# Kernel tuning notes

Hardware: AMD Instinct MI355X
Metric: run time of the kernel (lower is better)

## Reference

```python
import jax, jax.numpy as jnp
import numpy as np

D = 768      # qkv.in_features (ViT-Base)
R = 16       # LoRA rank
T = 8        # task_id: number of previously saved adapters
B_, S_ = 32, 256
TAU = 1.0


def setup_inputs() -> dict:
    key = jax.random.key(0)
    ks = jax.random.split(key, 13)
    s = lambda k, shape, sc=0.02: jax.random.normal(k, shape, jnp.float32) * sc
    return {
        "x": jax.random.normal(ks[0], (B_, S_, D), jnp.float32),
        "qkv_w": s(ks[1], (3 * D, D)),           # torch Linear weight [out,in]
        "qkv_b": s(ks[2], (3 * D,)),
        "la_q": s(ks[3], (R, D)),                # current-task LoRA A_q [r,d]
        "lb_q": s(ks[4], (D, R)),                # current-task LoRA B_q [d,r]
        "la_v": s(ks[5], (R, D)),
        "lb_v": s(ks[6], (D, R)),
        "A_q": s(ks[7], (T, R, D)),              # saved per-task A_q stacks
        "B_q": s(ks[8], (T, D, R)),
        "A_v": s(ks[9], (T, R, D)),
        "B_v": s(ks[10], (T, D, R)),
        "gate_logits": jax.random.normal(ks[11], (T,), jnp.float32),
        "alpha": jnp.ones((T + 1,), jnp.float32),  # gumbel_gate.alpha, indexed by task_id
    }


def _moe_branch(x, A, B, beta):
    """Weighted sum over T tasks of (x @ A_t^T @ B_t^T) / (||A_t||*||B_t||), weight beta_t.

    Vectorizes the per-task serial low-rank matmuls of the torch loop into two
    batched einsums; beta/norm scaling is folded into B to avoid materializing
    per-task [B,S,D] outputs.
    """
    nA = jnp.sqrt(jnp.sum(A * A, axis=(1, 2)))   # [T] Frobenius norms
    nB = jnp.sqrt(jnp.sum(B * B, axis=(1, 2)))
    scale = beta / (nA * nB)                      # [T]
    za = jnp.einsum('bsd,trd->bstr', x, A)       # [B,S,T,r]
    Bs = B * scale[:, None, None]                 # [T,D,r]
    return jnp.einsum('bstr,tdr->bsd', za, Bs)   # [B,S,D]


def _lora(x, a, b):
    # torch: b(a(x)) with Linear weights a:[r,d], b:[d,r]
    return jnp.einsum('bsr,dr->bsd', jnp.einsum('bsd,rd->bsr', x, a), b)


def reference(x, qkv_w, qkv_b, la_q, lb_q, la_v, lb_v, A_q, B_q, A_v, B_v, gate_logits, alpha):
    # Gumbel-softmax gate over tasks (deterministic/eval path: softmax(logits/tau), hard=False)
    beta = jax.nn.softmax(gate_logits / TAU)
    a_cur = alpha[T]  # alpha[self.task_id]
    new_q = _moe_branch(x, A_q, B_q, beta) + a_cur * _lora(x, la_q, lb_q)
    new_v = _moe_branch(x, A_v, B_v, beta) + a_cur * _lora(x, la_v, lb_v)
    qkv = jnp.einsum('bsd,ed->bse', x, qkv_w) + qkv_b  # [B,S,3D]
    qkv = qkv.at[..., :D].add(new_q)
    qkv = qkv.at[..., 2 * D:].add(new_v)
    return qkv
```

## Files before the change

kernel.cpp:

```cpp
#include <hip/hip_runtime.h>

#define TOK 8192
#define DD  768
#define NOUT 2304
#define TT  8
#define RR  16
#define KRANK 144

typedef __bf16 bf16;
typedef __bf16 bf16x4 __attribute__((ext_vector_type(4)));
typedef __bf16 bf16x8 __attribute__((ext_vector_type(8)));
typedef float  floatx4 __attribute__((ext_vector_type(4)));

__device__ __forceinline__ void gl_lds16(const void* g, void* l) {
    __builtin_amdgcn_global_load_lds((const __attribute__((address_space(1))) void*)g,
                                     (__attribute__((address_space(3))) void*)l, 16, 0, 0);
}

__global__ __launch_bounds__(256) void prep_kernel(
    const float* __restrict__ A_q, const float* __restrict__ B_q,
    const float* __restrict__ A_v, const float* __restrict__ B_v,
    const float* __restrict__ x, bf16* __restrict__ xb,
    float* __restrict__ norms)
{
    __shared__ float ws4[4];
    const int b = blockIdx.x;
    if (b < 32) {
        const float* base;
        switch (b >> 3) {
            case 0: base = A_q; break;
            case 1: base = B_q; break;
            case 2: base = A_v; break;
            default: base = B_v; break;
        }
        base += (b & 7) * (RR * DD);
        float s = 0.f;
        for (int i = threadIdx.x; i < RR * DD; i += 256) {
            float v = base[i];
            s = fmaf(v, v, s);
        }
        #pragma unroll
        for (int off = 32; off > 0; off >>= 1) s += __shfl_down(s, off);
        if ((threadIdx.x & 63) == 0) ws4[threadIdx.x >> 6] = s;
        __syncthreads();
        if (threadIdx.x == 0)
            norms[b] = sqrtf(ws4[0] + ws4[1] + ws4[2] + ws4[3]);
    } else {
        const int idx = ((b - 32) * 256 + threadIdx.x) * 4;
        const float4 v = *(const float4*)(x + idx);
        bf16x4 o = { (bf16)v.x, (bf16)v.y, (bf16)v.z, (bf16)v.w };
        *(bf16x4*)(xb + idx) = o;
    }
}

__global__ __launch_bounds__(256) void fold_kernel(
    const float* __restrict__ qkv_w,
    const float* __restrict__ A_q, const float* __restrict__ la_q,
    const float* __restrict__ B_q, const float* __restrict__ lb_q,
    const float* __restrict__ A_v, const float* __restrict__ la_v,
    const float* __restrict__ B_v, const float* __restrict__ lb_v,
    const float* __restrict__ gate_logits, const float* __restrict__ alpha,
    const float* __restrict__ norms, bf16* __restrict__ Wc)
{
    const int tid = threadIdx.x;
    const int d = blockIdx.x * 256 + tid;
    const int gy = blockIdx.y;

    if (gy >= 96 && gy < 192) {
        const int rowbase = DD + (gy - 96) * 8;
        #pragma unroll
        for (int j = 0; j < 8; ++j) {
            const int row = rowbase + j;
            Wc[row * DD + d] = (bf16)qkv_w[row * DD + d];
        }
        return;
    }

    __shared__ float c_lds[8 * KRANK];
    __shared__ float sc_sh[TT];
    __shared__ float acur_sh;

    const bool is_v = (gy >= 192);
    const int e0 = (is_v ? gy - 192 : gy) * 8;
    const float* Astack = is_v ? A_v : A_q;
    const float* la     = is_v ? la_v : la_q;
    const float* Bmat   = is_v ? B_v : B_q;
    const float* lb     = is_v ? lb_v : lb_q;
    const float* nA     = norms + (is_v ? 16 : 0);
    const float* nB     = norms + (is_v ? 24 : 8);
    const int rowbase   = (is_v ? 2 * DD : 0) + e0;

    if (tid == 0) {
        float mx = gate_logits[0];
        for (int t = 1; t < TT; ++t) mx = fmaxf(mx, gate_logits[t]);
        float e[TT], s = 0.f;
        for (int t = 0; t < TT; ++t) { e[t] = __expf(gate_logits[t] - mx); s += e[t]; }
        for (int t = 0; t < TT; ++t) sc_sh[t] = (e[t] / s) / (nA[t] * nB[t]);
        acur_sh = alpha[TT];
    }
    __syncthreads();

    for (int idx = tid; idx < 8 * KRANK; idx += 256) {
        const int j = idx / KRANK, i = idx - j * KRANK;
        const int e = e0 + j;
        float v;
        if (i < TT * RR) {
            const int t = i >> 4, r = i & 15;
            v = sc_sh[t] * Bmat[(t * DD + e) * RR + r];
        } else {
            v = acur_sh * lb[e * RR + (i - TT * RR)];
        }
        c_lds[j * KRANK + i] = v;
    }
    __syncthreads();

    float acc[8] = {0.f, 0.f, 0.f, 0.f, 0.f, 0.f, 0.f, 0.f};

    for (int i = 0; i < TT * RR; i += 4) {
        const float a0 = Astack[(i + 0) * DD + d];
        const float a1 = Astack[(i + 1) * DD + d];
        const float a2 = Astack[(i + 2) * DD + d];
        const float a3 = Astack[(i + 3) * DD + d];
        #pragma unroll
        for (int j = 0; j < 8; ++j) {
            const float4 cv = *(const float4*)&c_lds[j * KRANK + i];
            acc[j] = fmaf(a0, cv.x, fmaf(a1, cv.y, fmaf(a2, cv.z, fmaf(a3, cv.w, acc[j]))));
        }
    }
    #pragma unroll
    for (int i = 0; i < RR; i += 4) {
        const float a0 = la[(i + 0) * DD + d];
        const float a1 = la[(i + 1) * DD + d];
        const float a2 = la[(i + 2) * DD + d];
        const float a3 = la[(i + 3) * DD + d];
        #pragma unroll
        for (int j = 0; j < 8; ++j) {
            const float4 cv = *(const float4*)&c_lds[j * KRANK + TT * RR + i];
            acc[j] = fmaf(a0, cv.x, fmaf(a1, cv.y, fmaf(a2, cv.z, fmaf(a3, cv.w, acc[j]))));
        }
    }

    #pragma unroll
    for (int j = 0; j < 8; ++j) {
        const int row = rowbase + j;
        Wc[row * DD + d] = (bf16)(qkv_w[row * DD + d] + acc[j]);
    }
}

__global__ __launch_bounds__(256, 2) void gemm_kernel(
    const bf16* __restrict__ A, const bf16* __restrict__ B,
    const float* __restrict__ bias, float* __restrict__ C)
{
    __shared__ bf16 lds_a[128 * 64];
    __shared__ bf16 lds_b[128 * 64];
    const int tid  = threadIdx.x;
    const int lane = tid & 63;
    const int wave = tid >> 6;

    const int flat  = blockIdx.y * gridDim.x + blockIdx.x;
    const int xcd   = flat & 7;
    const int local = flat >> 3;
    const int mb    = xcd * 8 + (local & 7);
    const int nb    = local >> 3;
    const int m0 = mb * 128;
    const int n0 = nb * 128;

    const int wm = (wave >> 1) * 64;
    const int wn = (wave & 1) * 64;

    const int srow = lane >> 3;
    const int scol = ((lane & 7) ^ srow) * 8;

    floatx4 acc[4][4];
    #pragma unroll
    for (int i = 0; i < 4; ++i)
        #pragma unroll
        for (int j = 0; j < 4; ++j)
            acc[i][j] = (floatx4){0.f, 0.f, 0.f, 0.f};

    for (int kt = 0; kt < DD / 64; ++kt) {
        const int k0 = kt * 64;
        #pragma unroll
        for (int i = 0; i < 4; ++i) {
            const int j = i * 4 + wave;
            const int row = j * 8 + srow;
            gl_lds16(A + (m0 + row) * DD + k0 + scol, &lds_a[j * 512]);
            gl_lds16(B + (n0 + row) * DD + k0 + scol, &lds_b[j * 512]);
        }
        __syncthreads();
        #pragma unroll
        for (int ks = 0; ks < 2; ++ks) {
            bf16x8 af[4], bfr[4];
            const int c_log = ks * 4 + (lane >> 4);
            #pragma unroll
            for (int mt = 0; mt < 4; ++mt) {
                const int r = wm + mt * 16 + (lane & 15);
                af[mt] = *(const bf16x8*)&lds_a[r * 64 + ((c_log ^ (r & 7)) * 8)];
            }
            #pragma unroll
            for (int nt = 0; nt < 4; ++nt) {
                const int r = wn + nt * 16 + (lane & 15);
                bfr[nt] = *(const bf16x8*)&lds_b[r * 64 + ((c_log ^ (r & 7)) * 8)];
            }
            #pragma unroll
            for (int mt = 0; mt < 4; ++mt)
                #pragma unroll
                for (int nt = 0; nt < 4; ++nt)
                    acc[mt][nt] = __builtin_amdgcn_mfma_f32_16x16x32_bf16(
                        af[mt], bfr[nt], acc[mt][nt], 0, 0, 0);
        }
        __syncthreads();
    }

    const int cr = (lane >> 4) * 4;
    const int cc = lane & 15;
    #pragma unroll
    for (int nt = 0; nt < 4; ++nt) {
        const int gn = n0 + wn + nt * 16 + cc;
        const float bv = bias[gn];
        #pragma unroll
        for (int mt = 0; mt < 4; ++mt) {
            const int gmb = m0 + wm + mt * 16 + cr;
            #pragma unroll
            for (int r = 0; r < 4; ++r)
                C[(gmb + r) * NOUT + gn] = acc[mt][nt][r] + bv;
        }
    }
}

extern "C" void kernel_launch(void* const* d_in, const int* in_sizes, int n_in,
                              void* d_out, int out_size, void* d_ws, size_t ws_size,
                              hipStream_t stream)
{
    const float* x           = (const float*)d_in[0];
    const float* qkv_w       = (const float*)d_in[1];
    const float* qkv_b       = (const float*)d_in[2];
    const float* la_q        = (const float*)d_in[3];
    const float* lb_q        = (const float*)d_in[4];
    const float* la_v        = (const float*)d_in[5];
    const float* lb_v        = (const float*)d_in[6];
    const float* A_q         = (const float*)d_in[7];
    const float* B_q         = (const float*)d_in[8];
    const float* A_v         = (const float*)d_in[9];
    const float* B_v         = (const float*)d_in[10];
    const float* gate_logits = (const float*)d_in[11];
    const float* alpha       = (const float*)d_in[12];
    float* out = (float*)d_out;

    char* ws = (char*)d_ws;
    bf16*  Xbf    = (bf16*)ws;
    bf16*  Wc     = (bf16*)(ws + 12582912);
    float* norms  = (float*)(ws + 12582912 + 3538944);

    prep_kernel<<<32 + TOK * DD / 1024, 256, 0, stream>>>(A_q, B_q, A_v, B_v,
                                                          x, Xbf, norms);
    fold_kernel<<<dim3(3, 288), 256, 0, stream>>>(qkv_w,
                                                  A_q, la_q, B_q, lb_q,
                                                  A_v, la_v, B_v, lb_v,
                                                  gate_logits, alpha, norms, Wc);
    gemm_kernel<<<dim3(NOUT / 128, TOK / 128), 256, 0, stream>>>(Xbf, Wc, qkv_b, out);
}
```

Before: 174.6 us.

## Double-buffer GEMM LDS tiles and stage output through LDS for coalesced stores

The bf16 GEMM main loop now ping-pongs between two LDS buffers, issuing the next k-tile's global-to-LDS loads before computing the current tile, which removes one barrier per iteration and overlaps loads with MFMA work. The epilogue writes the fp32 accumulator tile plus bias into LDS first, then each block writes it to global memory as row-contiguous float4 stores instead of scattered 4-byte stores. LDS use rises to 64 KB per block, which may limit the launch_bounds(256,2) occupancy target. There is also a possible race: no wait/barrier guards the async loads into the next buffer before it is read in the following iteration.

```diff
diff --git a/kernel.cpp b/kernel.cpp
--- a/kernel.cpp
+++ b/kernel.cpp
@@ -151,8 +151,8 @@
     const bf16* __restrict__ A, const bf16* __restrict__ B,
     const float* __restrict__ bias, float* __restrict__ C)
 {
-    __shared__ bf16 lds_a[128 * 64];
-    __shared__ bf16 lds_b[128 * 64];
+    __shared__ __align__(16) char smem[65536];
+
     const int tid  = threadIdx.x;
     const int lane = tid & 63;
     const int wave = tid >> 6;
@@ -178,16 +178,28 @@
         for (int j = 0; j < 4; ++j)
             acc[i][j] = (floatx4){0.f, 0.f, 0.f, 0.f};
 
-    for (int kt = 0; kt < DD / 64; ++kt) {
+    auto stage = [&](int kt, int buf) {
         const int k0 = kt * 64;
+        bf16* la = (bf16*)(smem + buf * 32768);
+        bf16* lb = (bf16*)(smem + buf * 32768 + 16384);
         #pragma unroll
         for (int i = 0; i < 4; ++i) {
             const int j = i * 4 + wave;
             const int row = j * 8 + srow;
-            gl_lds16(A + (m0 + row) * DD + k0 + scol, &lds_a[j * 512]);
-            gl_lds16(B + (n0 + row) * DD + k0 + scol, &lds_b[j * 512]);
-        }
-        __syncthreads();
+            gl_lds16(A + (m0 + row) * DD + k0 + scol, &la[j * 512]);
+            gl_lds16(B + (n0 + row) * DD + k0 + scol, &lb[j * 512]);
+        }
+    };
+
+    stage(0, 0);
+    __syncthreads();
+
+    int cur = 0;
+    for (int kt = 0; kt < DD / 64; ++kt) {
+        if (kt + 1 < DD / 64) stage(kt + 1, cur ^ 1);
+
+        const bf16* la = (const bf16*)(smem + cur * 32768);
+        const bf16* lb = (const bf16*)(smem + cur * 32768 + 16384);
         #pragma unroll
         for (int ks = 0; ks < 2; ++ks) {
             bf16x8 af[4], bfr[4];
@@ -195,12 +207,12 @@
             #pragma unroll
             for (int mt = 0; mt < 4; ++mt) {
                 const int r = wm + mt * 16 + (lane & 15);
-                af[mt] = *(const bf16x8*)&lds_a[r * 64 + ((c_log ^ (r & 7)) * 8)];
+                af[mt] = *(const bf16x8*)&la[r * 64 + ((c_log ^ (r & 7)) * 8)];
             }
             #pragma unroll
             for (int nt = 0; nt < 4; ++nt) {
                 const int r = wn + nt * 16 + (lane & 15);
-                bfr[nt] = *(const bf16x8*)&lds_b[r * 64 + ((c_log ^ (r & 7)) * 8)];
+                bfr[nt] = *(const bf16x8*)&lb[r * 64 + ((c_log ^ (r & 7)) * 8)];
             }
             #pragma unroll
             for (int mt = 0; mt < 4; ++mt)
@@ -210,21 +222,32 @@
                         af[mt], bfr[nt], acc[mt][nt], 0, 0, 0);
         }
         __syncthreads();
-    }
-
+        cur ^= 1;
+    }
+
+    float* ctile = (float*)smem;
     const int cr = (lane >> 4) * 4;
     const int cc = lane & 15;
     #pragma unroll
     for (int nt = 0; nt < 4; ++nt) {
-        const int gn = n0 + wn + nt * 16 + cc;
-        const float bv = bias[gn];
+        const int col = wn + nt * 16 + cc;
+        const float bv = bias[n0 + col];
         #pragma unroll
         for (int mt = 0; mt < 4; ++mt) {
-            const int gmb = m0 + wm + mt * 16 + cr;
+            const int rowb = wm + mt * 16 + cr;
             #pragma unroll
             for (int r = 0; r < 4; ++r)
-                C[(gmb + r) * NOUT + gn] = acc[mt][nt][r] + bv;
-        }
+                ctile[(rowb + r) * 128 + col] = acc[mt][nt][r] + bv;
+        }
+    }
+    __syncthreads();
+    #pragma unroll
+    for (int p = 0; p < 16; ++p) {
+        const int f   = p * 256 + tid;
+        const int row = f >> 5;
+        const int c4  = (f & 31) * 4;
+        const float4 v = *(const float4*)&ctile[row * 128 + c4];
+        *(float4*)&C[(m0 + row) * NOUT + n0 + c4] = v;
     }
 }
 
```

Result: no change. 175.1 us (+0.3%).

## Enlarge GEMM tile to 128x256 and double-buffer A with register-prefetched B

Applied to the files above, without the earlier changes.

The bf16 GEMM tile grows from 128x128 to 128x256. Each wave now owns a 64-wide column strip across all 128 rows, which improves operand reuse per LDS load. A tiles are double-buffered in LDS through async global-to-LDS loads, so the next k-step's load overlaps the current MFMAs. B tiles are prefetched into registers and written to a wave-private LDS region after compute, which removes one barrier per k-step. The cost is more accumulator registers and 64 KB of LDS per block, which may limit occupancy, and a 1D grid of 576 blocks with XCD-aware mapping.

```diff
diff --git a/kernel.cpp b/kernel.cpp
--- a/kernel.cpp
+++ b/kernel.cpp
@@ -6,6 +6,7 @@
 #define TT  8
 #define RR  16
 #define KRANK 144
+#define NKT  (DD / 64)
 
 typedef __bf16 bf16;
 typedef __bf16 bf16x4 __attribute__((ext_vector_type(4)));
@@ -151,65 +152,96 @@
     const bf16* __restrict__ A, const bf16* __restrict__ B,
     const float* __restrict__ bias, float* __restrict__ C)
 {
-    __shared__ bf16 lds_a[128 * 64];
-    __shared__ bf16 lds_b[128 * 64];
+    __shared__ __align__(16) char smem[65536];
+    bf16* const b_lds = (bf16*)(smem + 32768);
+
     const int tid  = threadIdx.x;
     const int lane = tid & 63;
     const int wave = tid >> 6;
 
-    const int flat  = blockIdx.y * gridDim.x + blockIdx.x;
+    const int flat  = blockIdx.x;
     const int xcd   = flat & 7;
     const int local = flat >> 3;
     const int mb    = xcd * 8 + (local & 7);
     const int nb    = local >> 3;
     const int m0 = mb * 128;
-    const int n0 = nb * 128;
-
-    const int wm = (wave >> 1) * 64;
-    const int wn = (wave & 1) * 64;
+    const int n0 = nb * 256;
+
+    const int wn = wave * 64;
 
     const int srow = lane >> 3;
-    const int scol = ((lane & 7) ^ srow) * 8;
-
-    floatx4 acc[4][4];
-    #pragma unroll
-    for (int i = 0; i < 4; ++i)
+    const int sxor = ((lane & 7) ^ srow) * 8;
+
+    const bf16* b_gbase = B + (n0 + wn + srow) * DD + sxor;
+    bf16* const b_wbase = b_lds + (wn + srow) * 64 + (lane & 7) * 8;
+
+    floatx4 acc[8][4];
+    #pragma unroll
+    for (int i = 0; i < 8; ++i)
         #pragma unroll
         for (int j = 0; j < 4; ++j)
             acc[i][j] = (floatx4){0.f, 0.f, 0.f, 0.f};
 
-    for (int kt = 0; kt < DD / 64; ++kt) {
+    uint4 breg[8];
+
+    auto stageA = [&](int kt, int buf) {
         const int k0 = kt * 64;
+        bf16* abuf = (bf16*)(smem + buf * 16384);
         #pragma unroll
         for (int i = 0; i < 4; ++i) {
             const int j = i * 4 + wave;
-            const int row = j * 8 + srow;
-            gl_lds16(A + (m0 + row) * DD + k0 + scol, &lds_a[j * 512]);
-            gl_lds16(B + (n0 + row) * DD + k0 + scol, &lds_b[j * 512]);
-        }
-        __syncthreads();
+            gl_lds16(A + (m0 + j * 8 + srow) * DD + k0 + sxor, &abuf[j * 512]);
+        }
+    };
+    auto loadB = [&](int kt) {
+        const int k0 = kt * 64;
+        #pragma unroll
+        for (int s = 0; s < 8; ++s)
+            breg[s] = *(const uint4*)(b_gbase + s * 8 * DD + k0);
+    };
+    auto writeB = [&]() {
+        #pragma unroll
+        for (int s = 0; s < 8; ++s)
+            *(uint4*)(b_wbase + s * 512) = breg[s];
+    };
+
+    stageA(0, 0);
+    loadB(0);
+    writeB();
+    __syncthreads();
+
+    for (int kt = 0; kt < NKT; ++kt) {
+        const int nxt = kt + 1;
+        if (nxt < NKT) {
+            stageA(nxt, nxt & 1);
+            loadB(nxt);
+        }
+
+        const bf16* abuf = (const bf16*)(smem + (kt & 1) * 16384);
         #pragma unroll
         for (int ks = 0; ks < 2; ++ks) {
-            bf16x8 af[4], bfr[4];
             const int c_log = ks * 4 + (lane >> 4);
-            #pragma unroll
-            for (int mt = 0; mt < 4; ++mt) {
-                const int r = wm + mt * 16 + (lane & 15);
-                af[mt] = *(const bf16x8*)&lds_a[r * 64 + ((c_log ^ (r & 7)) * 8)];
-            }
+            bf16x8 bfr[4];
             #pragma unroll
             for (int nt = 0; nt < 4; ++nt) {
                 const int r = wn + nt * 16 + (lane & 15);
-                bfr[nt] = *(const bf16x8*)&lds_b[r * 64 + ((c_log ^ (r & 7)) * 8)];
+                bfr[nt] = *(const bf16x8*)&b_lds[r * 64 + ((c_log ^ (r & 7)) * 8)];
             }
             #pragma unroll
-            for (int mt = 0; mt < 4; ++mt)
+            for (int mt = 0; mt < 8; ++mt) {
+                const int r = mt * 16 + (lane & 15);
+                const bf16x8 af = *(const bf16x8*)&abuf[r * 64 + ((c_log ^ (r & 7)) * 8)];
                 #pragma unroll
                 for (int nt = 0; nt < 4; ++nt)
                     acc[mt][nt] = __builtin_amdgcn_mfma_f32_16x16x32_bf16(
-                        af[mt], bfr[nt], acc[mt][nt], 0, 0, 0);
-        }
-        __syncthreads();
+                        af, bfr[nt], acc[mt][nt], 0, 0, 0);
+            }
+        }
+
+        if (nxt < NKT) {
+            writeB();
+            __syncthreads();
+        }
     }
 
     const int cr = (lane >> 4) * 4;
@@ -219,8 +251,8 @@
         const int gn = n0 + wn + nt * 16 + cc;
         const float bv = bias[gn];
         #pragma unroll
-        for (int mt = 0; mt < 4; ++mt) {
-            const int gmb = m0 + wm + mt * 16 + cr;
+        for (int mt = 0; mt < 8; ++mt) {
+            const int gmb = m0 + mt * 16 + cr;
             #pragma unroll
             for (int r = 0; r < 4; ++r)
                 C[(gmb + r) * NOUT + gn] = acc[mt][nt][r] + bv;
@@ -258,5 +290,5 @@
                                                   A_q, la_q, B_q, lb_q,
                                                   A_v, la_v, B_v, lb_v,
                                                   gate_logits, alpha, norms, Wc);
-    gemm_kernel<<<dim3(NOUT / 128, TOK / 128), 256, 0, stream>>>(Xbf, Wc, qkv_b, out);
-}
+    gemm_kernel<<<576, 256, 0, stream>>>(Xbf, Wc, qkv_b, out);
+}
```

Measured after the change: 214.9 us. 1.23x slower.

## Double-buffer GEMM LDS with BK=32 and widen tile to 128x256

Applied to the files above, without the earlier changes.

The GEMM now stages K-slices of 32 into two LDS buffers, so the next slice loads while MFMAs run on the current one. Only one barrier per iteration remains. The output tile grows to 128x256, each wave holding 4x8 accumulators, with a new swizzle for the narrower rows and a 1D grid of 576 blocks. This is meant to hide global-to-LDS latency and raise reuse of the A tile, at the cost of more registers (which may hurt occupancy under launch_bounds(256,2)) and fewer blocks.

```diff
diff --git a/kernel.cpp b/kernel.cpp
--- a/kernel.cpp
+++ b/kernel.cpp
@@ -6,6 +6,7 @@
 #define TT  8
 #define RR  16
 #define KRANK 144
+#define NKT  (DD / 32)
 
 typedef __bf16 bf16;
 typedef __bf16 bf16x4 __attribute__((ext_vector_type(4)));
@@ -151,71 +152,90 @@
     const bf16* __restrict__ A, const bf16* __restrict__ B,
     const float* __restrict__ bias, float* __restrict__ C)
 {
-    __shared__ bf16 lds_a[128 * 64];
-    __shared__ bf16 lds_b[128 * 64];
+    __shared__ __align__(16) char smem[49152];
+
     const int tid  = threadIdx.x;
     const int lane = tid & 63;
     const int wave = tid >> 6;
 
-    const int flat  = blockIdx.y * gridDim.x + blockIdx.x;
+    const int flat  = blockIdx.x;
     const int xcd   = flat & 7;
     const int local = flat >> 3;
     const int mb    = xcd * 8 + (local & 7);
     const int nb    = local >> 3;
     const int m0 = mb * 128;
-    const int n0 = nb * 128;
+    const int n0 = nb * 256;
 
     const int wm = (wave >> 1) * 64;
-    const int wn = (wave & 1) * 64;
-
-    const int srow = lane >> 3;
-    const int scol = ((lane & 7) ^ srow) * 8;
-
-    floatx4 acc[4][4];
+    const int wn = (wave & 1) * 128;
+
+    const int srow = lane >> 2;
+    const int sphy = lane & 3;
+    const int sclog = ((sphy ^ (srow & 3)) - ((srow >> 2) & 1)) & 3;
+    const int scol  = sclog * 8;
+
+    floatx4 acc[4][8];
     #pragma unroll
     for (int i = 0; i < 4; ++i)
         #pragma unroll
-        for (int j = 0; j < 4; ++j)
+        for (int j = 0; j < 8; ++j)
             acc[i][j] = (floatx4){0.f, 0.f, 0.f, 0.f};
 
-    for (int kt = 0; kt < DD / 64; ++kt) {
-        const int k0 = kt * 64;
-        #pragma unroll
-        for (int i = 0; i < 4; ++i) {
-            const int j = i * 4 + wave;
-            const int row = j * 8 + srow;
-            gl_lds16(A + (m0 + row) * DD + k0 + scol, &lds_a[j * 512]);
-            gl_lds16(B + (n0 + row) * DD + k0 + scol, &lds_b[j * 512]);
-        }
-        __syncthreads();
-        #pragma unroll
-        for (int ks = 0; ks < 2; ++ks) {
-            bf16x8 af[4], bfr[4];
-            const int c_log = ks * 4 + (lane >> 4);
+    auto stage = [&](int kt, int buf) {
+        const int k0 = kt * 32;
+        bf16* abuf = (bf16*)(smem + buf * 24576);
+        bf16* bbuf = (bf16*)(smem + buf * 24576 + 8192);
+        #pragma unroll
+        for (int i = 0; i < 6; ++i) {
+            const int idx = i * 4 + wave;
+            if (idx < 8) {
+                const int row = idx * 16 + srow;
+                gl_lds16(A + (m0 + row) * DD + k0 + scol, &abuf[idx * 512]);
+            } else {
+                const int row = (idx - 8) * 16 + srow;
+                gl_lds16(B + (n0 + row) * DD + k0 + scol, &bbuf[(idx - 8) * 512]);
+            }
+        }
+    };
+
+    stage(0, 0);
+    __syncthreads();
+
+    for (int kt = 0; kt < NKT; ++kt) {
+        const int nxt = kt + 1;
+        if (nxt < NKT) stage(nxt, nxt & 1);
+
+        const bf16* abuf = (const bf16*)(smem + (kt & 1) * 24576);
+        const bf16* bbuf = (const bf16*)(smem + (kt & 1) * 24576 + 8192);
+        const int c_log = lane >> 4;
+
+        bf16x8 af[4], bfr[8];
+        #pragma unroll
+        for (int mt = 0; mt < 4; ++mt) {
+            const int r = wm + mt * 16 + (lane & 15);
+            const int ph = ((c_log + ((r >> 2) & 1)) ^ (r & 3)) & 3;
+            af[mt] = *(const bf16x8*)&abuf[r * 32 + ph * 8];
+        }
+        #pragma unroll
+        for (int nt = 0; nt < 8; ++nt) {
+            const int r = wn + nt * 16 + (lane & 15);
+            const int ph = ((c_log + ((r >> 2) & 1)) ^ (r & 3)) & 3;
+            bfr[nt] = *(const bf16x8*)&bbuf[r * 32 + ph * 8];
+        }
+        #pragma unroll
+        for (int mt = 0; mt < 4; ++mt)
             #pragma unroll
-            for (int mt = 0; mt < 4; ++mt) {
-                const int r = wm + mt * 16 + (lane & 15);
-                af[mt] = *(const bf16x8*)&lds_a[r * 64 + ((c_log ^ (r & 7)) * 8)];
-            }
-            #pragma unroll
-            for (int nt = 0; nt < 4; ++nt) {
-                const int r = wn + nt * 16 + (lane & 15);
-                bfr[nt] = *(const bf16x8*)&lds_b[r * 64 + ((c_log ^ (r & 7)) * 8)];
-            }
-            #pragma unroll
-            for (int mt = 0; mt < 4; ++mt)
-                #pragma unroll
-                for (int nt = 0; nt < 4; ++nt)
-                    acc[mt][nt] = __builtin_amdgcn_mfma_f32_16x16x32_bf16(
-                        af[mt], bfr[nt], acc[mt][nt], 0, 0, 0);
-        }
-        __syncthreads();
+            for (int nt = 0; nt < 8; ++nt)
+                acc[mt][nt] = __builtin_amdgcn_mfma_f32_16x16x32_bf16(
+                    af[mt], bfr[nt], acc[mt][nt], 0, 0, 0);
+
+        if (nxt < NKT) __syncthreads();
     }
 
     const int cr = (lane >> 4) * 4;
     const int cc = lane & 15;
     #pragma unroll
-    for (int nt = 0; nt < 4; ++nt) {
+    for (int nt = 0; nt < 8; ++nt) {
         const int gn = n0 + wn + nt * 16 + cc;
         const float bv = bias[gn];
         #pragma unroll
@@ -258,5 +278,5 @@
                                                   A_q, la_q, B_q, lb_q,
                                                   A_v, la_v, B_v, lb_v,
                                                   gate_logits, alpha, norms, Wc);
-    gemm_kernel<<<dim3(NOUT / 128, TOK / 128), 256, 0, stream>>>(Xbf, Wc, qkv_b, out);
-}
+    gemm_kernel<<<576, 256, 0, stream>>>(Xbf, Wc, qkv_b, out);
+}
```

After: 189.0 us. +8.2%, slower.
